# Optimization experiments

Measured on AMD Instinct MI355X. Metric: run time of the kernel, lower is better.

## Reference

```python
import jax, jax.numpy as jnp
import numpy as np

B, C, Q, E = 32, 1024, 128, 512

def setup_inputs() -> dict:
    key = jax.random.key(0)
    k1, k2, k3 = jax.random.split(key, 3)
    context = jax.random.normal(k1, (B, C, E), dtype=jnp.float32)
    question = jax.random.normal(k2, (B, Q, E), dtype=jnp.float32)
    # ws = [ws_q | ws_c | ws_m], matching cat([q, ctx, q*ctx]) order
    ws = jax.random.normal(k3, (3 * E,), dtype=jnp.float32) * (1.0 / np.sqrt(E))
    return {"context": context, "question": question, "ws": ws}

def reference(context, question, ws):
    ws_q, ws_c, ws_m = ws[:E], ws[E:2 * E], ws[2 * E:]
    # similarity[b,c,q] = ws_q.q[b,q] + ws_c.c[b,c] + ws_m.(q[b,q]*c[b,c])
    sim = (jnp.einsum('bqe,e->bq', question, ws_q)[:, None, :]
           + jnp.einsum('bce,e->bc', context, ws_c)[:, :, None]
           + jnp.einsum('bce,bqe,e->bcq', context, question, ws_m))  # (B,C,Q)
    c2q = jnp.einsum('bcq,bqe->bce', jax.nn.softmax(sim, axis=2), question)  # (B,C,E)
    q2c_w = jax.nn.softmax(jnp.max(sim, axis=2), axis=1)  # (B,C)
    q2c = jnp.einsum('bc,bce->be', q2c_w, context)[:, None, :]  # (B,1,E)
    return (c2q, q2c)
```

## Files before the change

kernel.cpp:

```cpp
#include <hip/hip_runtime.h>

#define BB 32
#define CC 1024
#define QQ 128
#define EE 512

typedef unsigned int uint32;
typedef unsigned short u16;
typedef __bf16 bf16x8 __attribute__((ext_vector_type(8)));
typedef float f32x4 __attribute__((ext_vector_type(4)));

#define QMF_OFF  (0u)
#define QTF_OFF  (4u<<20)
#define QDP_OFF  (8u<<20)
#define RDEN_OFF ((8u<<20)+(64u<<10))
#define MB_OFF   ((8u<<20)+(192u<<10))
#define SB_OFF   ((8u<<20)+(200u<<10))
#define PVB_OFF  ((8u<<20)+(256u<<10))
#define P_OFF    (13u<<20)

__device__ __forceinline__ u16 bfc(float f){
  __bf16 h = (__bf16)f;
  return __builtin_bit_cast(u16, h);
}
__device__ __forceinline__ float bf2f(uint32 lo16){
  return __builtin_bit_cast(float, lo16 << 16);
}

__global__ __launch_bounds__(256) void k_prep(const float* __restrict__ q,
                                              const float* __restrict__ ws,
                                              unsigned char* __restrict__ wsp){
  const int b = blockIdx.x >> 2, et = blockIdx.x & 3, e0 = et*128;
  __shared__ u16 tm[128*136];
  __shared__ u16 tt[128*136];
  const int tid = threadIdx.x;
  float* qdp = (float*)(wsp + QDP_OFF) + (size_t)(b*4 + et)*128;
  #pragma unroll
  for (int i=0;i<16;i++){
    int id = tid + i*256;
    int qi = id >> 5;
    int el = (id & 31) << 2;
    float4 v = *(const float4*)(q + (size_t)(b*QQ+qi)*EE + e0 + el);
    float4 a = *(const float4*)(ws +          e0 + el);
    float4 c = *(const float4*)(ws +   EE +   e0 + el);
    float4 m = *(const float4*)(ws + 2*EE +   e0 + el);
    ushort4 um; um.x = bfc(v.x*m.x + c.x); um.y = bfc(v.y*m.y + c.y);
                um.z = bfc(v.z*m.z + c.z); um.w = bfc(v.w*m.w + c.w);
    *(ushort4*)&tm[qi*136 + el] = um;
    ushort4 ut; ut.x = bfc(v.x); ut.y = bfc(v.y); ut.z = bfc(v.z); ut.w = bfc(v.w);
    *(ushort4*)&tt[qi*136 + el] = ut;
    float d = v.x*a.x + v.y*a.y + v.z*a.z + v.w*a.w;
    d += __shfl_xor(d,1); d += __shfl_xor(d,2); d += __shfl_xor(d,4);
    d += __shfl_xor(d,8); d += __shfl_xor(d,16);
    if ((tid & 31) == 0) qdp[qi] = d;
  }
  __syncthreads();
  const int lane = tid & 63, wv = tid >> 6, l15 = lane & 15, l4 = lane >> 4;
  uint4* qmf = (uint4*)(wsp + QMF_OFF);
  uint4* qtf = (uint4*)(wsp + QTF_OFF);
  #pragma unroll
  for (int i=0;i<8;i++){
    int f = wv*8 + i;
    int kl = f >> 3, nf = f & 7;
    uint4 u = *(const uint4*)&tm[(nf*16 + l15)*136 + kl*32 + l4*8];
    qmf[(size_t)((b*16 + et*4 + kl)*8 + nf)*64 + lane] = u;
  }
  #pragma unroll
  for (int i=0;i<8;i++){
    int f = wv*8 + i;
    int ks2 = f >> 3, nl = f & 7, ne = et*8 + nl;
    uint32 x[4];
    #pragma unroll
    for (int p=0;p<4;p++){
      u16 t0 = tt[(ks2*32 + l4*8 + 2*p    )*136 + nl*16 + l15];
      u16 t1 = tt[(ks2*32 + l4*8 + 2*p + 1)*136 + nl*16 + l15];
      x[p] = (uint32)t0 | ((uint32)t1 << 16);
    }
    uint4 u; u.x = x[0]; u.y = x[1]; u.z = x[2]; u.w = x[3];
    qtf[(size_t)((b*4 + ks2)*32 + ne)*64 + lane] = u;
  }
}

__global__ __launch_bounds__(512, 4) void k_sim(const float* __restrict__ ctx,
                                                unsigned char* __restrict__ wsp){
  __shared__ __align__(16) unsigned char buf[16384];
  __shared__ float mx_s[16*8];
  __shared__ float sm_s[16*8];
  __shared__ float wrow_s[16];

  const int bid = blockIdx.x;
  const int sw  = (bid & 7)*256 + (bid >> 3);
  const int b   = sw >> 6;
  const int t   = sw & 63;
  const int tid = threadIdx.x;
  const int lane = tid & 63;
  const int w    = tid >> 6;
  const int l15  = lane & 15;
  const int l4   = lane >> 4;

  const float4* cb4 = (const float4*)(ctx + (size_t)(b*CC + t*16)*EE);
  float4 v[4];
  #pragma unroll
  for (int i=0;i<4;i++) v[i] = cb4[i*512 + tid];

  float qdv[4];
  {
    const float* qdp = (const float*)(wsp + QDP_OFF) + (size_t)b*512;
    #pragma unroll
    for (int r=0;r<4;r++){
      const int qi = w*16 + l4*4 + r;
      qdv[r] = qdp[qi] + qdp[128+qi] + qdp[256+qi] + qdp[384+qi];
    }
  }

  {
    const int colb = (tid & 127)*8;
    #pragma unroll
    for (int i=0;i<4;i++){
      const int row = i*4 + (tid >> 7);
      uint2 u;
      u.x = (uint32)bfc(v[i].x) | ((uint32)bfc(v[i].y) << 16);
      u.y = (uint32)bfc(v[i].z) | ((uint32)bfc(v[i].w) << 16);
      *(uint2*)(buf + row*1024 + (colb ^ ((row & 7) << 4))) = u;
    }
  }
  __syncthreads();

  const uint4* qmf4 = (const uint4*)(wsp + QMF_OFF);
  f32x4 acc = (f32x4){0.f,0.f,0.f,0.f};
  #pragma unroll
  for (int ks=0; ks<16; ks++){
    bf16x8 a = __builtin_bit_cast(bf16x8, qmf4[(size_t)((b*16 + ks)*8 + w)*64 + lane]);
    bf16x8 bf = __builtin_bit_cast(bf16x8,
      *(const uint4*)(buf + l15*1024 + ((ks*64 + l4*16) ^ ((l15 & 7) << 4))));
    acc = __builtin_amdgcn_mfma_f32_16x16x32_bf16(a, bf, acc, 0, 0, 0);
  }

  {
    float m = -3.0e38f, s = 0.f;
    u16 hb[4];
    #pragma unroll
    for (int r=0;r<4;r++){
      float vv = fminf(acc[r] + qdv[r], 80.f);
      m = fmaxf(m, vv);
      u16 h = bfc(__expf(vv));
      hb[r] = h;
      s += bf2f(h);
    }
    uint2 u; u.x = (uint32)hb[0] | ((uint32)hb[1]<<16);
             u.y = (uint32)hb[2] | ((uint32)hb[3]<<16);
    *(uint2*)(wsp + P_OFF
      + ((size_t)(b*64 + t)*4 + (w>>1))*1024
      + (((2*w + (l4>>1)) & 3)*16 + l15)*16 + (l4&1)*8) = u;
    m = fmaxf(m, __shfl_xor(m, 16)); m = fmaxf(m, __shfl_xor(m, 32));
    s += __shfl_xor(s, 16);          s += __shfl_xor(s, 32);
    if (l4 == 0){ mx_s[l15*8 + w] = m; sm_s[l15*8 + w] = s; }
  }
  __syncthreads();

  if (tid < 16){
    const float* sp = &sm_s[tid*8];
    float sum = sp[0]+sp[1]+sp[2]+sp[3]+sp[4]+sp[5]+sp[6]+sp[7];
    ((float*)(wsp + RDEN_OFF))[b*1024 + t*16 + tid] = 1.f/sum;
    const float* mp = &mx_s[tid*8];
    float mf = fmaxf(fmaxf(fmaxf(mp[0],mp[1]),fmaxf(mp[2],mp[3])),
                     fmaxf(fmaxf(mp[4],mp[5]),fmaxf(mp[6],mp[7])));
    float M = mf;
    M = fmaxf(M, __shfl_xor(M,1)); M = fmaxf(M, __shfl_xor(M,2));
    M = fmaxf(M, __shfl_xor(M,4)); M = fmaxf(M, __shfl_xor(M,8));
    float wr = __expf(mf - M);
    wrow_s[tid] = wr;
    float S = wr;
    S += __shfl_xor(S,1); S += __shfl_xor(S,2);
    S += __shfl_xor(S,4); S += __shfl_xor(S,8);
    if (tid == 0){
      ((float*)(wsp + MB_OFF))[b*64 + t] = M;
      ((float*)(wsp + SB_OFF))[b*64 + t] = S;
    }
  }
  __syncthreads();

  {
    float pv = 0.f;
    #pragma unroll
    for (int rr=0; rr<16; rr++){
      uint32 x = *(const u16*)(buf + rr*1024 + ((tid*2) ^ ((rr & 7) << 4)));
      pv = fmaf(wrow_s[rr], bf2f(x), pv);
    }
    ((float*)(wsp + PVB_OFF))[(size_t)(b*64 + t)*512 + tid] = pv;
  }
}

__global__ __launch_bounds__(256, 4) void k_out(unsigned char* __restrict__ wsp,
                                                float* __restrict__ out){
  __shared__ __align__(16) unsigned char qts[32768];
  __shared__ float sc_s[64];
  __shared__ float dinv_s;

  const int bid = blockIdx.x;
  const int tid = threadIdx.x;

  if (bid >= 2048){
    const int b = bid - 2048;
    if (tid < 64){
      float Mk = ((const float*)(wsp + MB_OFF))[b*64 + tid];
      float Sk = ((const float*)(wsp + SB_OFF))[b*64 + tid];
      float M = Mk;
      M = fmaxf(M, __shfl_xor(M,1));  M = fmaxf(M, __shfl_xor(M,2));
      M = fmaxf(M, __shfl_xor(M,4));  M = fmaxf(M, __shfl_xor(M,8));
      M = fmaxf(M, __shfl_xor(M,16)); M = fmaxf(M, __shfl_xor(M,32));
      float ev = __expf(Mk - M);
      float d = ev*Sk;
      d += __shfl_xor(d,1);  d += __shfl_xor(d,2);  d += __shfl_xor(d,4);
      d += __shfl_xor(d,8);  d += __shfl_xor(d,16); d += __shfl_xor(d,32);
      sc_s[tid] = ev;
      if (tid == 0) dinv_s = 1.f/d;
    }
    __syncthreads();
    const float* pvb = (const float*)(wsp + PVB_OFF) + (size_t)b*64*512;
    float a0 = 0.f, a1 = 0.f;
    #pragma unroll 8
    for (int k=0;k<64;k++){
      float s = sc_s[k];
      a0 = fmaf(s, pvb[(size_t)k*512 + tid],       a0);
      a1 = fmaf(s, pvb[(size_t)k*512 + tid + 256], a1);
    }
    size_t base = (size_t)BB*CC*EE + (size_t)b*EE;
    float di = dinv_s;
    out[base + tid]       = a0*di;
    out[base + tid + 256] = a1*di;
    return;
  }

  const int sw  = (bid & 7)*256 + (bid >> 3);
  const int b   = sw >> 6;
  const int rr  = sw & 63;
  const int ct  = rr >> 2;
  const int et  = rr & 3;
  const int lane = tid & 63;
  const int w    = tid >> 6;
  const int l15  = lane & 15;
  const int l4   = lane >> 4;

  const unsigned char* qtfb = wsp + QTF_OFF + (size_t)b*131072;
  #pragma unroll
  for (int j=0;j<8;j++){
    __builtin_amdgcn_global_load_lds(
      (const __attribute__((address_space(1))) uint32*)
        (qtfb + (size_t)(w*32 + et*8 + j)*1024 + lane*16),
      (__attribute__((address_space(3))) uint32*)(qts + (w*8 + j)*1024), 16, 0, 0);
  }

  bf16x8 pa[4];
  #pragma unroll
  for (int k2=0;k2<4;k2++)
    pa[k2] = __builtin_bit_cast(bf16x8,
      *(const uint4*)(wsp + P_OFF + ((size_t)(b*64 + ct*4 + w)*4 + k2)*1024 + lane*16));
  float rden[4];
  {
    const float* rg = (const float*)(wsp + RDEN_OFF) + b*1024 + ct*64 + w*16;
    #pragma unroll
    for (int r=0;r<4;r++) rden[r] = rg[l4*4 + r];
  }
  __syncthreads();

  f32x4 acc2[8];
  #pragma unroll
  for (int n=0;n<8;n++) acc2[n] = (f32x4){0.f,0.f,0.f,0.f};
  #pragma unroll
  for (int k2=0;k2<4;k2++){
    #pragma unroll
    for (int n=0;n<8;n++){
      bf16x8 bq = __builtin_bit_cast(bf16x8,
        *(const uint4*)(qts + (k2*8 + n)*1024 + lane*16));
      acc2[n] = __builtin_amdgcn_mfma_f32_16x16x32_bf16(pa[k2], bq, acc2[n], 0, 0, 0);
    }
  }

  float* ob = out + (size_t)(b*CC + ct*64 + w*16)*EE + et*128;
  #pragma unroll
  for (int n=0;n<8;n++){
    #pragma unroll
    for (int r=0;r<4;r++)
      ob[(size_t)(l4*4 + r)*EE + n*16 + l15] = acc2[n][r]*rden[r];
  }
}

extern "C" void kernel_launch(void* const* d_in, const int* in_sizes, int n_in,
                              void* d_out, int out_size, void* d_ws, size_t ws_size,
                              hipStream_t stream){
  const float* ctx = (const float*)d_in[0];
  const float* q   = (const float*)d_in[1];
  const float* ws  = (const float*)d_in[2];
  float* out = (float*)d_out;
  unsigned char* wsp = (unsigned char*)d_ws;

  k_prep<<<dim3(BB*4),    dim3(256), 0, stream>>>(q, ws, wsp);
  k_sim <<<dim3(2048),    dim3(512), 0, stream>>>(ctx, wsp);
  k_out <<<dim3(2048+32), dim3(256), 0, stream>>>(wsp, out);
}
```

Before: 54.68 us.

## Load context via async global-to-LDS as fp32 and fold softmax normalization into P

```diff
diff --git a/kernel.cpp b/kernel.cpp
--- a/kernel.cpp
+++ b/kernel.cpp
@@ -13,7 +13,6 @@
 #define QMF_OFF  (0u)
 #define QTF_OFF  (4u<<20)
 #define QDP_OFF  (8u<<20)
-#define RDEN_OFF ((8u<<20)+(64u<<10))
 #define MB_OFF   ((8u<<20)+(192u<<10))
 #define SB_OFF   ((8u<<20)+(200u<<10))
 #define PVB_OFF  ((8u<<20)+(256u<<10))
@@ -83,7 +82,7 @@
 
 __global__ __launch_bounds__(512, 4) void k_sim(const float* __restrict__ ctx,
                                                 unsigned char* __restrict__ wsp){
-  __shared__ __align__(16) unsigned char buf[16384];
+  __shared__ __align__(16) unsigned char buf[32768];
   __shared__ float mx_s[16*8];
   __shared__ float sm_s[16*8];
   __shared__ float wrow_s[16];
@@ -98,10 +97,19 @@
   const int l15  = lane & 15;
   const int l4   = lane >> 4;
 
-  const float4* cb4 = (const float4*)(ctx + (size_t)(b*CC + t*16)*EE);
-  float4 v[4];
-  #pragma unroll
-  for (int i=0;i<4;i++) v[i] = cb4[i*512 + tid];
+  {
+    const unsigned char* cb = (const unsigned char*)(ctx + (size_t)(b*CC + t*16)*EE);
+    #pragma unroll
+    for (int j=0;j<4;j++){
+      const int chunk = w*4 + j;
+      const int row   = chunk >> 1;
+      const int gs    = ((chunk & 1)*64 + lane) ^ (row & 7);
+      __builtin_amdgcn_global_load_lds(
+        (const __attribute__((address_space(1))) uint32*)(cb + row*2048 + gs*16),
+        (__attribute__((address_space(3))) uint32*)(buf + chunk*1024 + lane*16),
+        16, 0, 0);
+    }
+  }
 
   float qdv[4];
   {
@@ -112,56 +120,56 @@
       qdv[r] = qdp[qi] + qdp[128+qi] + qdp[256+qi] + qdp[384+qi];
     }
   }
-
-  {
-    const int colb = (tid & 127)*8;
-    #pragma unroll
-    for (int i=0;i<4;i++){
-      const int row = i*4 + (tid >> 7);
-      uint2 u;
-      u.x = (uint32)bfc(v[i].x) | ((uint32)bfc(v[i].y) << 16);
-      u.y = (uint32)bfc(v[i].z) | ((uint32)bfc(v[i].w) << 16);
-      *(uint2*)(buf + row*1024 + (colb ^ ((row & 7) << 4))) = u;
-    }
-  }
   __syncthreads();
 
   const uint4* qmf4 = (const uint4*)(wsp + QMF_OFF);
   f32x4 acc = (f32x4){0.f,0.f,0.f,0.f};
-  #pragma unroll
-  for (int ks=0; ks<16; ks++){
-    bf16x8 a = __builtin_bit_cast(bf16x8, qmf4[(size_t)((b*16 + ks)*8 + w)*64 + lane]);
-    bf16x8 bf = __builtin_bit_cast(bf16x8,
-      *(const uint4*)(buf + l15*1024 + ((ks*64 + l4*16) ^ ((l15 & 7) << 4))));
-    acc = __builtin_amdgcn_mfma_f32_16x16x32_bf16(a, bf, acc, 0, 0, 0);
-  }
-
+  {
+    const int swz = l15 & 7;
+    const unsigned char* rowb = buf + l15*2048;
+    #pragma unroll
+    for (int ks=0; ks<16; ks++){
+      bf16x8 a = __builtin_bit_cast(bf16x8, qmf4[(size_t)((b*16 + ks)*8 + w)*64 + lane]);
+      const int gs0 = ks*8 + l4*2;
+      float4 x = *(const float4*)(rowb + ((gs0    ) ^ swz)*16);
+      float4 y = *(const float4*)(rowb + ((gs0 + 1) ^ swz)*16);
+      bf16x8 bf;
+      bf[0]=(__bf16)x.x; bf[1]=(__bf16)x.y; bf[2]=(__bf16)x.z; bf[3]=(__bf16)x.w;
+      bf[4]=(__bf16)y.x; bf[5]=(__bf16)y.y; bf[6]=(__bf16)y.z; bf[7]=(__bf16)y.w;
+      acc = __builtin_amdgcn_mfma_f32_16x16x32_bf16(a, bf, acc, 0, 0, 0);
+    }
+  }
+
+  float p[4];
   {
     float m = -3.0e38f, s = 0.f;
-    u16 hb[4];
     #pragma unroll
     for (int r=0;r<4;r++){
       float vv = fminf(acc[r] + qdv[r], 80.f);
       m = fmaxf(m, vv);
-      u16 h = bfc(__expf(vv));
-      hb[r] = h;
-      s += bf2f(h);
-    }
+      p[r] = __expf(vv);
+      s += p[r];
+    }
+    m = fmaxf(m, __shfl_xor(m, 16)); m = fmaxf(m, __shfl_xor(m, 32));
+    s += __shfl_xor(s, 16);          s += __shfl_xor(s, 32);
+    if (l4 == 0){ mx_s[l15*8 + w] = m; sm_s[l15*8 + w] = s; }
+  }
+  __syncthreads();
+
+  {
+    const float* sp = &sm_s[l15*8];
+    const float rden = 1.f/(sp[0]+sp[1]+sp[2]+sp[3]+sp[4]+sp[5]+sp[6]+sp[7]);
+    u16 hb[4];
+    #pragma unroll
+    for (int r=0;r<4;r++) hb[r] = bfc(p[r]*rden);
     uint2 u; u.x = (uint32)hb[0] | ((uint32)hb[1]<<16);
              u.y = (uint32)hb[2] | ((uint32)hb[3]<<16);
     *(uint2*)(wsp + P_OFF
       + ((size_t)(b*64 + t)*4 + (w>>1))*1024
       + (((2*w + (l4>>1)) & 3)*16 + l15)*16 + (l4&1)*8) = u;
-    m = fmaxf(m, __shfl_xor(m, 16)); m = fmaxf(m, __shfl_xor(m, 32));
-    s += __shfl_xor(s, 16);          s += __shfl_xor(s, 32);
-    if (l4 == 0){ mx_s[l15*8 + w] = m; sm_s[l15*8 + w] = s; }
-  }
-  __syncthreads();
+  }
 
   if (tid < 16){
-    const float* sp = &sm_s[tid*8];
-    float sum = sp[0]+sp[1]+sp[2]+sp[3]+sp[4]+sp[5]+sp[6]+sp[7];
-    ((float*)(wsp + RDEN_OFF))[b*1024 + t*16 + tid] = 1.f/sum;
     const float* mp = &mx_s[tid*8];
     float mf = fmaxf(fmaxf(fmaxf(mp[0],mp[1]),fmaxf(mp[2],mp[3])),
                      fmaxf(fmaxf(mp[4],mp[5]),fmaxf(mp[6],mp[7])));
@@ -181,11 +189,12 @@
   __syncthreads();
 
   {
+    const int sl = tid >> 2, in = (tid & 3)*4;
     float pv = 0.f;
     #pragma unroll
     for (int rr=0; rr<16; rr++){
-      uint32 x = *(const u16*)(buf + rr*1024 + ((tid*2) ^ ((rr & 7) << 4)));
-      pv = fmaf(wrow_s[rr], bf2f(x), pv);
+      float x = *(const float*)(buf + rr*2048 + ((sl ^ (rr & 7))*16) + in);
+      pv = fmaf(wrow_s[rr], x, pv);
     }
     ((float*)(wsp + PVB_OFF))[(size_t)(b*64 + t)*512 + tid] = pv;
   }
@@ -256,12 +265,6 @@
   for (int k2=0;k2<4;k2++)
     pa[k2] = __builtin_bit_cast(bf16x8,
       *(const uint4*)(wsp + P_OFF + ((size_t)(b*64 + ct*4 + w)*4 + k2)*1024 + lane*16));
-  float rden[4];
-  {
-    const float* rg = (const float*)(wsp + RDEN_OFF) + b*1024 + ct*64 + w*16;
-    #pragma unroll
-    for (int r=0;r<4;r++) rden[r] = rg[l4*4 + r];
-  }
   __syncthreads();
 
   f32x4 acc2[8];
@@ -282,7 +285,7 @@
   for (int n=0;n<8;n++){
     #pragma unroll
     for (int r=0;r<4;r++)
-      ob[(size_t)(l4*4 + r)*EE + n*16 + l15] = acc2[n][r]*rden[r];
+      ob[(size_t)(l4*4 + r)*EE + n*16 + l15] = acc2[n][r];
   }
 }
 
```

Measured after the change: 53.09 us. -2.9%, faster.
